# Performance work log

Hardware: AMD Instinct MI355X
Metric: run time of the kernel (lower is better)

## Reference

```python
import jax, jax.numpy as jnp
import numpy as np

H = 1024
N_HEADS = 16
DK = H // N_HEADS
B = 4
S_TGT = 1024
S_SRC = 1024
LN_EPS = 1e-5


def _ln(x, g, b):
    m = jnp.mean(x, axis=-1, keepdims=True)
    v = jnp.mean(jnp.square(x - m), axis=-1, keepdims=True)
    return (x - m) * jax.lax.rsqrt(v + LN_EPS) * g + b


def _mha(q_in, k_in, v_in, wq, wk, wv, wo, mask):
    # Equivalent to torch split(hidden//n_splits)+cat(dim=0) head layout:
    # per-(batch,head) scaled dot-product attention.
    Bq, Sq, _ = q_in.shape
    Sk = k_in.shape[1]
    q = (q_in @ wq).reshape(Bq, Sq, N_HEADS, DK)
    k = (k_in @ wk).reshape(Bq, Sk, N_HEADS, DK)
    v = (v_in @ wv).reshape(Bq, Sk, N_HEADS, DK)
    scores = jnp.einsum('bqhd,bkhd->bhqk', q, k)
    if mask is not None:
        scores = jnp.where(mask[:, None, :, :], -jnp.inf, scores)
    attn = jax.nn.softmax(scores / np.sqrt(DK).astype(np.float32), axis=-1)
    ctx = jnp.einsum('bhqk,bkhd->bqhd', attn, v).reshape(Bq, Sq, H)
    return ctx @ wo


def setup_inputs() -> dict:
    key = jax.random.key(0)
    ks = jax.random.split(key, 16)
    std = 1.0 / np.sqrt(H)
    p = {
        'x': jax.random.normal(ks[0], (B, S_TGT, H), jnp.float32),
        'key_and_value': jax.random.normal(ks[1], (B, S_SRC, H), jnp.float32),
        'mask': jnp.zeros((B, S_TGT, S_SRC), jnp.bool_),  # no padding
        # causal mask: True above the diagonal (masked positions)
        'future_mask': jnp.broadcast_to(
            jnp.triu(jnp.ones((S_TGT, S_TGT), jnp.bool_), k=1), (B, S_TGT, S_TGT)),
        'sa_wq': jax.random.normal(ks[2], (H, H), jnp.float32) * std,
        'sa_wk': jax.random.normal(ks[3], (H, H), jnp.float32) * std,
        'sa_wv': jax.random.normal(ks[4], (H, H), jnp.float32) * std,
        'sa_wo': jax.random.normal(ks[5], (H, H), jnp.float32) * std,
        'ca_wq': jax.random.normal(ks[6], (H, H), jnp.float32) * std,
        'ca_wk': jax.random.normal(ks[7], (H, H), jnp.float32) * std,
        'ca_wv': jax.random.normal(ks[8], (H, H), jnp.float32) * std,
        'ca_wo': jax.random.normal(ks[9], (H, H), jnp.float32) * std,
        'fc_w1': jax.random.normal(ks[10], (H, 4 * H), jnp.float32) * std,
        'fc_b1': jnp.zeros((4 * H,), jnp.float32),
        'fc_w2': jax.random.normal(ks[11], (4 * H, H), jnp.float32) * (0.5 * std),
        'fc_b2': jnp.zeros((H,), jnp.float32),
        'ln1_g': jnp.ones((H,), jnp.float32), 'ln1_b': jnp.zeros((H,), jnp.float32),
        'ln2_g': jnp.ones((H,), jnp.float32), 'ln2_b': jnp.zeros((H,), jnp.float32),
        'ln3_g': jnp.ones((H,), jnp.float32), 'ln3_b': jnp.zeros((H,), jnp.float32),
    }
    return p


def reference(x, key_and_value, mask, future_mask,
              sa_wq, sa_wk, sa_wv, sa_wo,
              ca_wq, ca_wk, ca_wv, ca_wo,
              fc_w1, fc_b1, fc_w2, fc_b2,
              ln1_g, ln1_b, ln2_g, ln2_b, ln3_g, ln3_b):
    # prev is None path (training); dropout in eval mode = identity.
    z = _ln(x, ln1_g, ln1_b)
    z = x + _mha(z, z, z, sa_wq, sa_wk, sa_wv, sa_wo, future_mask)
    nkv = _ln(key_and_value, ln2_g, ln2_b)
    z = z + _mha(_ln(z, ln2_g, ln2_b), nkv, nkv, ca_wq, ca_wk, ca_wv, ca_wo, mask)
    h = jax.nn.relu(_ln(z, ln3_g, ln3_b) @ fc_w1 + fc_b1)
    z = z + (h @ fc_w2 + fc_b2)
    return z
```

## Files before the change

kernel.cpp:

```cpp
#include <hip/hip_runtime.h>
#include <hip/hip_bf16.h>

typedef __attribute__((ext_vector_type(8))) short short8;
typedef __attribute__((ext_vector_type(4))) float f32x4;
using bf16 = __hip_bfloat16;

__device__ __forceinline__ void gload16(const void* g, void* l) {
  __builtin_amdgcn_global_load_lds(
      (const __attribute__((address_space(1))) void*)g,
      (__attribute__((address_space(3))) void*)l, 16, 0, 0);
}

__device__ __forceinline__ short f2bf(float f) {
  bf16 h = __float2bfloat16(f);
  short s;
  __builtin_memcpy(&s, &h, 2);
  return s;
}

__global__ __launch_bounds__(256)
void wtr8(const float* w0, const float* w1, const float* w2, const float* w3,
          const float* w4, const float* w5, const float* w6, const float* w7,
          bf16* __restrict__ Wout) {
  __shared__ float tile[32][33];
  const float* w;
  switch (blockIdx.z) {
    case 0: w = w0; break; case 1: w = w1; break;
    case 2: w = w2; break; case 3: w = w3; break;
    case 4: w = w4; break; case 5: w = w5; break;
    case 6: w = w6; break; default: w = w7; break;
  }
  bf16* wt = Wout + (size_t)blockIdx.z * 1024 * 1024;
  const int tx = threadIdx.x & 31, ty = threadIdx.x >> 5;
  const int c0 = blockIdx.x * 32, r0 = blockIdx.y * 32;
#pragma unroll
  for (int i = 0; i < 4; ++i)
    tile[ty * 4 + i][tx] = w[(size_t)(r0 + ty * 4 + i) * 1024 + c0 + tx];
  __syncthreads();
#pragma unroll
  for (int i = 0; i < 4; ++i) {
    const int cc = ty * 4 + i;
    wt[(size_t)(c0 + cc) * 1024 + r0 + tx] = __float2bfloat16(tile[tx][cc]);
  }
}

__global__ __launch_bounds__(256)
void wtr(const float* __restrict__ w, bf16* __restrict__ wt, int R, int C) {
  __shared__ float tile[32][33];
  const int tx = threadIdx.x & 31, ty = threadIdx.x >> 5;
  const int c0 = blockIdx.x * 32, r0 = blockIdx.y * 32;
#pragma unroll
  for (int i = 0; i < 4; ++i)
    tile[ty * 4 + i][tx] = w[(size_t)(r0 + ty * 4 + i) * C + c0 + tx];
  __syncthreads();
#pragma unroll
  for (int i = 0; i < 4; ++i) {
    const int cc = ty * 4 + i;
    wt[(size_t)(c0 + cc) * R + r0 + tx] = __float2bfloat16(tile[tx][cc]);
  }
}

__global__ __launch_bounds__(256)
void ln_k(const float* __restrict__ x, const float* __restrict__ g,
          const float* __restrict__ b, bf16* __restrict__ y) {
  const int row = blockIdx.x, t = threadIdx.x;
  const int wv = t >> 6, l = t & 63;
  const float4 v = reinterpret_cast<const float4*>(x + (size_t)row * 1024)[t];
  float s = v.x + v.y + v.z + v.w;
  float s2 = v.x * v.x + v.y * v.y + v.z * v.z + v.w * v.w;
#pragma unroll
  for (int m = 1; m < 64; m <<= 1) {
    s += __shfl_xor(s, m, 64);
    s2 += __shfl_xor(s2, m, 64);
  }
  __shared__ float ps[4], ps2[4];
  if (l == 0) { ps[wv] = s; ps2[wv] = s2; }
  __syncthreads();
  s = ps[0] + ps[1] + ps[2] + ps[3];
  s2 = ps2[0] + ps2[1] + ps2[2] + ps2[3];
  const float mean = s * (1.f / 1024.f);
  const float var = s2 * (1.f / 1024.f) - mean * mean;
  const float rs = rsqrtf(var + 1e-5f);
  const float4 gg = reinterpret_cast<const float4*>(g)[t];
  const float4 bb = reinterpret_cast<const float4*>(b)[t];
  ushort4 o;
  o.x = (unsigned short)f2bf((v.x - mean) * rs * gg.x + bb.x);
  o.y = (unsigned short)f2bf((v.y - mean) * rs * gg.y + bb.y);
  o.z = (unsigned short)f2bf((v.z - mean) * rs * gg.z + bb.z);
  o.w = (unsigned short)f2bf((v.w - mean) * rs * gg.w + bb.w);
  reinterpret_cast<ushort4*>(y + (size_t)row * 1024)[t] = o;
}

template <int BM, int EPI>
__global__ __launch_bounds__(256, 2)
void gemm_bt(const bf16* __restrict__ A, const bf16* __restrict__ BT,
             const float* bias, const float* res, void* outp,
             int M, int N, int K, bf16* vtp, int nv0) {
  constexpr int WM = BM / 32;
  constexpr int APASS = BM / 32;
  __shared__ alignas(16) short al[2][BM * 64];
  __shared__ alignas(16) short bl[2][128 * 64];
  const int t = threadIdx.x;
  const int gx = N >> 7;
  const int nwg = gridDim.x * gridDim.y;
  int id = blockIdx.y * gridDim.x + blockIdx.x;
  id = (id & 7) * (nwg >> 3) + (id >> 3);
  const int bx = id % gx, by = id / gx;
  const int m0 = by * BM, n0 = bx * 128;
  const int wv = t >> 6, l = t & 63, lr = l & 15, lk = l >> 4;
  const int wr = wv >> 1, wc = wv & 1;
  const int tr = t >> 3, tc = (t & 7) * 8;
  const int tcs = (((t & 7) ^ (tr & 7)) * 8);
  const int cro0 = ((lk ^ (lr & 7)) * 8);
  const int cro1 = (((4 + lk) ^ (lr & 7)) * 8);

  f32x4 acc[WM][4];
#pragma unroll
  for (int i = 0; i < WM; ++i)
#pragma unroll
    for (int j = 0; j < 4; ++j) acc[i][j] = (f32x4)0.f;

#define STAGE(buf, k0)                                                        \
  do {                                                                        \
    _Pragma("unroll") for (int it = 0; it < APASS; ++it) {                    \
      const int row = it * 32 + tr;                                           \
      gload16(A + (size_t)(m0 + row) * K + (k0) + tcs,                        \
              (char*)&al[buf][row * 64 + tc]);                                \
    }                                                                         \
    _Pragma("unroll") for (int it = 0; it < 4; ++it) {                        \
      const int row = it * 32 + tr;                                           \
      gload16(BT + (size_t)(n0 + row) * K + (k0) + tcs,                       \
              (char*)&bl[buf][row * 64 + tc]);                                \
    }                                                                         \
  } while (0)

#define COMPUTE(cur)                                                          \
  do {                                                                        \
    _Pragma("unroll") for (int ks = 0; ks < 2; ++ks) {                        \
      const int cro = ks ? cro1 : cro0;                                       \
      short8 af[WM], bfv[4];                                                  \
      _Pragma("unroll") for (int m = 0; m < WM; ++m) af[m] =                  \
          *reinterpret_cast<const short8*>(                                   \
              &al[cur][(wr * (BM / 2) + m * 16 + lr) * 64 + cro]);            \
      _Pragma("unroll") for (int n = 0; n < 4; ++n) bfv[n] =                  \
          *reinterpret_cast<const short8*>(                                   \
              &bl[cur][(wc * 64 + n * 16 + lr) * 64 + cro]);                  \
      _Pragma("unroll") for (int m = 0; m < WM; ++m)                          \
          _Pragma("unroll") for (int n = 0; n < 4; ++n) acc[m][n] =           \
              __builtin_amdgcn_mfma_f32_16x16x32_bf16(af[m], bfv[n],          \
                                                      acc[m][n], 0, 0, 0);    \
    }                                                                         \
  } while (0)

  const int nt = K >> 6;
  if constexpr (BM == 64) {
    STAGE(0, 0);
    STAGE(1, 64);
    for (int tk = 0; tk < nt; ++tk) {
      const int cur = tk & 1;
      if (tk < nt - 1)
        asm volatile("s_waitcnt vmcnt(6)" ::: "memory");
      else
        asm volatile("s_waitcnt vmcnt(0)" ::: "memory");
      __builtin_amdgcn_s_barrier();
      COMPUTE(cur);
      if (tk + 2 < nt) {
        asm volatile("s_waitcnt lgkmcnt(0)" ::: "memory");
        __builtin_amdgcn_s_barrier();
        STAGE(cur, (tk + 2) << 6);
      }
    }
  } else {
    STAGE(0, 0);
    asm volatile("s_waitcnt vmcnt(0)" ::: "memory");
    __syncthreads();
    for (int tk = 0; tk < nt; ++tk) {
      const int cur = tk & 1;
      if (tk + 1 < nt) STAGE(cur ^ 1, (tk + 1) << 6);
      COMPUTE(cur);
      asm volatile("s_waitcnt vmcnt(0)" ::: "memory");
      __syncthreads();
    }
  }
#undef STAGE
#undef COMPUTE

  const int r0 = m0 + wr * (BM / 2), c0 = n0 + wc * 64;
  if constexpr (EPI == 4) {
#pragma unroll
    for (int m = 0; m < WM; ++m) {
      const int rowb = r0 + m * 16 + lk * 4;
      const int bb = rowb >> 10, s0 = rowb & 1023;
#pragma unroll
      for (int n = 0; n < 4; ++n) {
        const int col = c0 + n * 16 + lr;
        if (col < nv0) {
#pragma unroll
          for (int r = 0; r < 4; ++r)
            ((bf16*)outp)[(size_t)(rowb + r) * nv0 + col] =
                __float2bfloat16(acc[m][n][r]);
        } else {
          ushort4 u;
          u.x = (unsigned short)f2bf(acc[m][n][0]);
          u.y = (unsigned short)f2bf(acc[m][n][1]);
          u.z = (unsigned short)f2bf(acc[m][n][2]);
          u.w = (unsigned short)f2bf(acc[m][n][3]);
          const size_t vidx = ((size_t)bb * 1024 + (col - nv0)) * 1024 + s0;
          *reinterpret_cast<ushort4*>(vtp + vidx) = u;
        }
      }
    }
  } else {
#pragma unroll
    for (int m = 0; m < WM; ++m)
#pragma unroll
      for (int n = 0; n < 4; ++n) {
        const int col = c0 + n * 16 + lr;
#pragma unroll
        for (int r = 0; r < 4; ++r) {
          const int row = r0 + m * 16 + lk * 4 + r;
          const size_t idx = (size_t)row * N + col;
          float v = acc[m][n][r];
          if (EPI == 0) {
            ((bf16*)outp)[idx] = __float2bfloat16(v);
          } else if (EPI == 1) {
            ((float*)outp)[idx] = res[idx] + v;
          } else if (EPI == 2) {
            v += bias[col];
            ((bf16*)outp)[idx] = __float2bfloat16(fmaxf(v, 0.f));
          } else {
            ((float*)outp)[idx] = res[idx] + v + bias[col];
          }
        }
      }
  }
}

template <bool CAUSAL>
__global__ __launch_bounds__(256, 2)
void flash8(const bf16* __restrict__ Qb, int ldq,
            const bf16* __restrict__ Kb, int ldk,
            const bf16* __restrict__ VTb, bf16* __restrict__ Ob) {
  __shared__ alignas(16) short kl[3][64 * 64];
  __shared__ alignas(16) short vl[3][64 * 64];
  __shared__ alignas(16) short pl[4][32 * 72];
  const int t = threadIdx.x, wv = t >> 6, l = t & 63, lr = l & 15, lk = l >> 4;
  const int raw = blockIdx.y * 8 + blockIdx.x;
  const int id = (raw & 7) * 64 + (raw >> 3);
  const int qb = id & 7, bh = id >> 3;
  const int b = bh >> 4, h = bh & 15;
  const size_t rowbase = (size_t)b * 1024;
  const int q0 = qb * 128 + wv * 32;
  const bf16* Vbase = VTb + (rowbase + h * 64) * 1024;

  const int tr = t >> 3;
  const int tcd = (t & 7) * 8;
  const int tcs = (((t & 7) ^ (tr & 7)) * 8);
  const int cro0 = ((lk ^ (lr & 7)) * 8);
  const int cro1 = (((4 + lk) ^ (lr & 7)) * 8);

  short8 qf[2][2];
#pragma unroll
  for (int m = 0; m < 2; ++m)
#pragma unroll
    for (int ks = 0; ks < 2; ++ks)
      qf[m][ks] = *reinterpret_cast<const short8*>(
          Qb + (rowbase + q0 + m * 16 + lr) * ldq + h * 64 + ks * 32 + lk * 8);

  short8 ones;
#pragma unroll
  for (int j = 0; j < 8; ++j) ones[j] = (short)0x3F80;

  f32x4 accO[2][4];
  f32x4 accL[2];
#pragma unroll
  for (int m = 0; m < 2; ++m) {
#pragma unroll
    for (int n = 0; n < 4; ++n) accO[m][n] = (f32x4)0.f;
    accL[m] = (f32x4)0.f;
  }

  const int ntb = CAUSAL ? (qb * 2 + 2) : 16;
  const int myLast = q0 >> 6;

#define FSTAGE(buf, kv0)                                                      \
  do {                                                                        \
    _Pragma("unroll") for (int it = 0; it < 2; ++it) {                        \
      const int row = it * 32 + tr;                                           \
      gload16(Kb + (rowbase + (kv0) + row) * ldk + h * 64 + tcs,              \
              (char*)&kl[buf][row * 64 + tcd]);                               \
    }                                                                         \
    _Pragma("unroll") for (int it = 0; it < 2; ++it) {                        \
      const int row = it * 32 + tr;                                           \
      gload16(Vbase + (size_t)row * 1024 + (kv0) + tcs,                       \
              (char*)&vl[buf][row * 64 + tcd]);                               \
    }                                                                         \
  } while (0)

  FSTAGE(0, 0);
  FSTAGE(1, 64);
  int cur = 0;
  for (int tk = 0; tk < ntb; ++tk) {
    if (tk < ntb - 1)
      asm volatile("s_waitcnt vmcnt(4)" ::: "memory");
    else
      asm volatile("s_waitcnt vmcnt(0)" ::: "memory");
    __builtin_amdgcn_s_barrier();
    if (tk + 2 < ntb) {
      int stg = cur + 2;
      if (stg >= 3) stg -= 3;
      FSTAGE(stg, (tk + 2) << 6);
    }
    if (!CAUSAL || tk <= myLast) {
      const int kv0 = tk * 64;
      const bool needmask = CAUSAL && (tk == myLast);
      f32x4 sa[2][4];
#pragma unroll
      for (int m = 0; m < 2; ++m)
#pragma unroll
        for (int n = 0; n < 4; ++n) sa[m][n] = (f32x4)0.f;
#pragma unroll
      for (int ks = 0; ks < 2; ++ks) {
        const int cro = ks ? cro1 : cro0;
        short8 kf[4];
#pragma unroll
        for (int n = 0; n < 4; ++n)
          kf[n] = *reinterpret_cast<const short8*>(
              &kl[cur][(n * 16 + lr) * 64 + cro]);
        __builtin_amdgcn_s_setprio(1);
#pragma unroll
        for (int m = 0; m < 2; ++m)
#pragma unroll
          for (int n = 0; n < 4; ++n)
            sa[m][n] = __builtin_amdgcn_mfma_f32_16x16x32_bf16(
                qf[m][ks], kf[n], sa[m][n], 0, 0, 0);
        __builtin_amdgcn_s_setprio(0);
      }
#pragma unroll
      for (int m = 0; m < 2; ++m) {
#pragma unroll
        for (int r = 0; r < 4; ++r) {
          const int row = q0 + m * 16 + lk * 4 + r;
          float s0 = sa[m][0][r] * 0.125f, s1 = sa[m][1][r] * 0.125f;
          float s2 = sa[m][2][r] * 0.125f, s3 = sa[m][3][r] * 0.125f;
          if (needmask) {
            if (kv0 + 0 + lr > row) s0 = -1e30f;
            if (kv0 + 16 + lr > row) s1 = -1e30f;
            if (kv0 + 32 + lr > row) s2 = -1e30f;
            if (kv0 + 48 + lr > row) s3 = -1e30f;
          }
          const float p0 = __expf(s0), p1 = __expf(s1);
          const float p2 = __expf(s2), p3 = __expf(s3);
          const int prow = m * 16 + lk * 4 + r;
          pl[wv][prow * 72 + lr + 0] = f2bf(p0);
          pl[wv][prow * 72 + lr + 16] = f2bf(p1);
          pl[wv][prow * 72 + lr + 32] = f2bf(p2);
          pl[wv][prow * 72 + lr + 48] = f2bf(p3);
        }
      }
#pragma unroll
      for (int ks = 0; ks < 2; ++ks) {
        const int cro = ks ? cro1 : cro0;
        short8 pf[2], vf[4];
#pragma unroll
        for (int m = 0; m < 2; ++m)
          pf[m] = *reinterpret_cast<const short8*>(
              &pl[wv][(m * 16 + lr) * 72 + ks * 32 + lk * 8]);
#pragma unroll
        for (int n = 0; n < 4; ++n)
          vf[n] = *reinterpret_cast<const short8*>(
              &vl[cur][(n * 16 + lr) * 64 + cro]);
        __builtin_amdgcn_s_setprio(1);
#pragma unroll
        for (int m = 0; m < 2; ++m) {
#pragma unroll
          for (int n = 0; n < 4; ++n)
            accO[m][n] = __builtin_amdgcn_mfma_f32_16x16x32_bf16(
                pf[m], vf[n], accO[m][n], 0, 0, 0);
          accL[m] = __builtin_amdgcn_mfma_f32_16x16x32_bf16(
              pf[m], ones, accL[m], 0, 0, 0);
        }
        __builtin_amdgcn_s_setprio(0);
      }
    }
    cur = (cur + 1 == 3) ? 0 : cur + 1;
  }
#undef FSTAGE

#pragma unroll
  for (int m = 0; m < 2; ++m)
#pragma unroll
    for (int n = 0; n < 4; ++n)
#pragma unroll
      for (int r = 0; r < 4; ++r) {
        const int row = q0 + m * 16 + lk * 4 + r;
        const int col = n * 16 + lr;
        const float o = accO[m][n][r] / accL[m][r];
        Ob[(rowbase + row) * 1024 + h * 64 + col] = __float2bfloat16(o);
      }
}

extern "C" void kernel_launch(void* const* d_in, const int* in_sizes, int n_in,
                              void* d_out, int out_size, void* d_ws,
                              size_t ws_size, hipStream_t stream) {
  const float* x = (const float*)d_in[0];
  const float* kv_in = (const float*)d_in[1];
  const float* sa_wq = (const float*)d_in[4];
  const float* sa_wk = (const float*)d_in[5];
  const float* sa_wv = (const float*)d_in[6];
  const float* sa_wo = (const float*)d_in[7];
  const float* ca_wq = (const float*)d_in[8];
  const float* ca_wk = (const float*)d_in[9];
  const float* ca_wv = (const float*)d_in[10];
  const float* ca_wo = (const float*)d_in[11];
  const float* fc_w1 = (const float*)d_in[12];
  const float* fc_b1 = (const float*)d_in[13];
  const float* fc_w2 = (const float*)d_in[14];
  const float* fc_b2 = (const float*)d_in[15];
  const float* ln1_g = (const float*)d_in[16];
  const float* ln1_b = (const float*)d_in[17];
  const float* ln2_g = (const float*)d_in[18];
  const float* ln2_b = (const float*)d_in[19];
  const float* ln3_g = (const float*)d_in[20];
  const float* ln3_b = (const float*)d_in[21];

  char* ws = (char*)d_ws;
  const size_t MB = 1024 * 1024;
  bf16* W = (bf16*)ws;
  bf16* w1T = W + 8 * MB;
  bf16* w2T = W + 12 * MB;
  float* z = (float*)(ws + 32 * MB);
  bf16* t0 = (bf16*)(ws + 48 * MB);
  bf16* qkvb = (bf16*)(ws + 56 * MB);
  bf16* vts = (bf16*)(ws + 72 * MB);
  bf16* kb = (bf16*)(ws + 80 * MB);
  bf16* vtc = (bf16*)(ws + 88 * MB);
  bf16* qb = (bf16*)(ws + 96 * MB);
  bf16* ctx = (bf16*)(ws + 104 * MB);
  bf16* kvln = (bf16*)(ws + 112 * MB);
  bf16* hb = (bf16*)(ws + 120 * MB);

  const dim3 B256(256);
  wtr8<<<dim3(32, 32, 8), B256, 0, stream>>>(sa_wq, sa_wk, sa_wv, sa_wo,
                                             ca_wq, ca_wk, ca_wv, ca_wo, W);
  wtr<<<dim3(128, 32), B256, 0, stream>>>(fc_w1, w1T, 1024, 4096);
  wtr<<<dim3(32, 128), B256, 0, stream>>>(fc_w2, w2T, 4096, 1024);

  ln_k<<<4096, B256, 0, stream>>>(x, ln1_g, ln1_b, t0);
  gemm_bt<128, 4><<<dim3(24, 32), B256, 0, stream>>>(
      t0, W, nullptr, nullptr, qkvb, 4096, 3072, 1024, vts, 2048);
  flash8<true><<<dim3(8, 64), B256, 0, stream>>>(
      qkvb, 2048, qkvb + 1024, 2048, vts, ctx);
  gemm_bt<64, 1><<<dim3(8, 64), B256, 0, stream>>>(
      ctx, W + 3 * MB, nullptr, x, z, 4096, 1024, 1024, nullptr, 0);

  ln_k<<<4096, B256, 0, stream>>>(kv_in, ln2_g, ln2_b, kvln);
  ln_k<<<4096, B256, 0, stream>>>(z, ln2_g, ln2_b, t0);
  gemm_bt<128, 4><<<dim3(16, 32), B256, 0, stream>>>(
      kvln, W + 5 * MB, nullptr, nullptr, kb, 4096, 2048, 1024, vtc, 1024);
  gemm_bt<64, 0><<<dim3(8, 64), B256, 0, stream>>>(
      t0, W + 4 * MB, nullptr, nullptr, qb, 4096, 1024, 1024, nullptr, 0);
  flash8<false><<<dim3(8, 64), B256, 0, stream>>>(
      qb, 1024, kb, 1024, vtc, ctx);
  gemm_bt<64, 1><<<dim3(8, 64), B256, 0, stream>>>(
      ctx, W + 7 * MB, nullptr, z, z, 4096, 1024, 1024, nullptr, 0);

  ln_k<<<4096, B256, 0, stream>>>(z, ln3_g, ln3_b, t0);
  gemm_bt<128, 2><<<dim3(32, 32), B256, 0, stream>>>(
      t0, w1T, fc_b1, nullptr, hb, 4096, 4096, 1024, nullptr, 0);
  gemm_bt<64, 3><<<dim3(8, 64), B256, 0, stream>>>(
      hb, w2T, fc_b2, z, d_out, 4096, 1024, 4096, nullptr, 0);
}
```

Measured before the change: 360.0 us.

## Split-K the second FFN GEMM and unify double-buffered GEMM pipeline

The FC2 GEMM (K=4096) now runs as a split-K over two halves via blockIdx.z, each writing fp32 partials. A new elementwise kernel sums the partials with the residual and bias. This raises wave count and parallelism for the long-K GEMM. The BM=128 GEMM path also switches to the two-stage prefetch pipeline used by BM=64, with a matching vmcnt. The cost is extra fp32 partial traffic plus one more kernel launch.

```diff
diff --git a/kernel.cpp b/kernel.cpp
--- a/kernel.cpp
+++ b/kernel.cpp
@@ -91,13 +91,29 @@
   reinterpret_cast<ushort4*>(y + (size_t)row * 1024)[t] = o;
 }
 
+__global__ __launch_bounds__(256)
+void ffn_add(const float4* __restrict__ p0, const float4* __restrict__ p1,
+             const float4* __restrict__ res, const float4* __restrict__ bias,
+             float4* __restrict__ out) {
+  const size_t i = (size_t)blockIdx.x * 256 + threadIdx.x;
+  const float4 a = p0[i], b = p1[i], r = res[i];
+  const float4 g = bias[i & 255];
+  float4 o;
+  o.x = a.x + b.x + r.x + g.x;
+  o.y = a.y + b.y + r.y + g.y;
+  o.z = a.z + b.z + r.z + g.z;
+  o.w = a.w + b.w + r.w + g.w;
+  out[i] = o;
+}
+
 template <int BM, int EPI>
 __global__ __launch_bounds__(256, 2)
 void gemm_bt(const bf16* __restrict__ A, const bf16* __restrict__ BT,
              const float* bias, const float* res, void* outp,
-             int M, int N, int K, bf16* vtp, int nv0) {
+             int M, int N, int K, int lda, bf16* vtp, int nv0) {
   constexpr int WM = BM / 32;
   constexpr int APASS = BM / 32;
+  constexpr int NLD = APASS + 4;
   __shared__ alignas(16) short al[2][BM * 64];
   __shared__ alignas(16) short bl[2][128 * 64];
   const int t = threadIdx.x;
@@ -114,6 +130,9 @@
   const int cro0 = ((lk ^ (lr & 7)) * 8);
   const int cro1 = (((4 + lk) ^ (lr & 7)) * 8);
 
+  const bf16* Ab = (EPI == 5) ? A + (size_t)blockIdx.z * K : A;
+  const bf16* BTb = (EPI == 5) ? BT + (size_t)blockIdx.z * K : BT;
+
   f32x4 acc[WM][4];
 #pragma unroll
   for (int i = 0; i < WM; ++i)
@@ -124,12 +143,12 @@
   do {                                                                        \
     _Pragma("unroll") for (int it = 0; it < APASS; ++it) {                    \
       const int row = it * 32 + tr;                                           \
-      gload16(A + (size_t)(m0 + row) * K + (k0) + tcs,                        \
+      gload16(Ab + (size_t)(m0 + row) * lda + (k0) + tcs,                     \
               (char*)&al[buf][row * 64 + tc]);                                \
     }                                                                         \
     _Pragma("unroll") for (int it = 0; it < 4; ++it) {                        \
       const int row = it * 32 + tr;                                           \
-      gload16(BT + (size_t)(n0 + row) * K + (k0) + tcs,                       \
+      gload16(BTb + (size_t)(n0 + row) * lda + (k0) + tcs,                    \
               (char*)&bl[buf][row * 64 + tc]);                                \
     }                                                                         \
   } while (0)
@@ -153,33 +172,24 @@
   } while (0)
 
   const int nt = K >> 6;
-  if constexpr (BM == 64) {
-    STAGE(0, 0);
-    STAGE(1, 64);
-    for (int tk = 0; tk < nt; ++tk) {
-      const int cur = tk & 1;
-      if (tk < nt - 1)
+  STAGE(0, 0);
+  STAGE(1, 64);
+  for (int tk = 0; tk < nt; ++tk) {
+    const int cur = tk & 1;
+    if (tk < nt - 1) {
+      if constexpr (NLD == 6)
         asm volatile("s_waitcnt vmcnt(6)" ::: "memory");
       else
-        asm volatile("s_waitcnt vmcnt(0)" ::: "memory");
+        asm volatile("s_waitcnt vmcnt(8)" ::: "memory");
+    } else {
+      asm volatile("s_waitcnt vmcnt(0)" ::: "memory");
+    }
+    __builtin_amdgcn_s_barrier();
+    COMPUTE(cur);
+    if (tk + 2 < nt) {
+      asm volatile("s_waitcnt lgkmcnt(0)" ::: "memory");
       __builtin_amdgcn_s_barrier();
-      COMPUTE(cur);
-      if (tk + 2 < nt) {
-        asm volatile("s_waitcnt lgkmcnt(0)" ::: "memory");
-        __builtin_amdgcn_s_barrier();
-        STAGE(cur, (tk + 2) << 6);
-      }
-    }
-  } else {
-    STAGE(0, 0);
-    asm volatile("s_waitcnt vmcnt(0)" ::: "memory");
-    __syncthreads();
-    for (int tk = 0; tk < nt; ++tk) {
-      const int cur = tk & 1;
-      if (tk + 1 < nt) STAGE(cur ^ 1, (tk + 1) << 6);
-      COMPUTE(cur);
-      asm volatile("s_waitcnt vmcnt(0)" ::: "memory");
-      __syncthreads();
+      STAGE(cur, (tk + 2) << 6);
     }
   }
 #undef STAGE
@@ -211,6 +221,8 @@
       }
     }
   } else {
+    float* po5 = nullptr;
+    if constexpr (EPI == 5) po5 = blockIdx.z ? (float*)vtp : (float*)outp;
 #pragma unroll
     for (int m = 0; m < WM; ++m)
 #pragma unroll
@@ -228,8 +240,10 @@
           } else if (EPI == 2) {
             v += bias[col];
             ((bf16*)outp)[idx] = __float2bfloat16(fmaxf(v, 0.f));
+          } else if (EPI == 3) {
+            ((float*)outp)[idx] = res[idx] + v + bias[col];
           } else {
-            ((float*)outp)[idx] = res[idx] + v + bias[col];
+            po5[idx] = v;
           }
         }
       }
@@ -439,6 +453,8 @@
   bf16* ctx = (bf16*)(ws + 104 * MB);
   bf16* kvln = (bf16*)(ws + 112 * MB);
   bf16* hb = (bf16*)(ws + 120 * MB);
+  float* part0 = (float*)(ws + 56 * MB);
+  float* part1 = (float*)(ws + 80 * MB);
 
   const dim3 B256(256);
   wtr8<<<dim3(32, 32, 8), B256, 0, stream>>>(sa_wq, sa_wk, sa_wv, sa_wo,
@@ -448,26 +464,32 @@
 
   ln_k<<<4096, B256, 0, stream>>>(x, ln1_g, ln1_b, t0);
   gemm_bt<128, 4><<<dim3(24, 32), B256, 0, stream>>>(
-      t0, W, nullptr, nullptr, qkvb, 4096, 3072, 1024, vts, 2048);
+      t0, W, nullptr, nullptr, qkvb, 4096, 3072, 1024, 1024, vts, 2048);
   flash8<true><<<dim3(8, 64), B256, 0, stream>>>(
       qkvb, 2048, qkvb + 1024, 2048, vts, ctx);
   gemm_bt<64, 1><<<dim3(8, 64), B256, 0, stream>>>(
-      ctx, W + 3 * MB, nullptr, x, z, 4096, 1024, 1024, nullptr, 0);
+      ctx, W + 3 * MB, nullptr, x, z, 4096, 1024, 1024, 1024, nullptr, 0);
 
   ln_k<<<4096, B256, 0, stream>>>(kv_in, ln2_g, ln2_b, kvln);
   ln_k<<<4096, B256, 0, stream>>>(z, ln2_g, ln2_b, t0);
   gemm_bt<128, 4><<<dim3(16, 32), B256, 0, stream>>>(
-      kvln, W + 5 * MB, nullptr, nullptr, kb, 4096, 2048, 1024, vtc, 1024);
+      kvln, W + 5 * MB, nullptr, nullptr, kb, 4096, 2048, 1024, 1024, vtc,
+      1024);
   gemm_bt<64, 0><<<dim3(8, 64), B256, 0, stream>>>(
-      t0, W + 4 * MB, nullptr, nullptr, qb, 4096, 1024, 1024, nullptr, 0);
+      t0, W + 4 * MB, nullptr, nullptr, qb, 4096, 1024, 1024, 1024, nullptr,
+      0);
   flash8<false><<<dim3(8, 64), B256, 0, stream>>>(
       qb, 1024, kb, 1024, vtc, ctx);
   gemm_bt<64, 1><<<dim3(8, 64), B256, 0, stream>>>(
-      ctx, W + 7 * MB, nullptr, z, z, 4096, 1024, 1024, nullptr, 0);
+      ctx, W + 7 * MB, nullptr, z, z, 4096, 1024, 1024, 1024, nullptr, 0);
 
   ln_k<<<4096, B256, 0, stream>>>(z, ln3_g, ln3_b, t0);
   gemm_bt<128, 2><<<dim3(32, 32), B256, 0, stream>>>(
-      t0, w1T, fc_b1, nullptr, hb, 4096, 4096, 1024, nullptr, 0);
-  gemm_bt<64, 3><<<dim3(8, 64), B256, 0, stream>>>(
-      hb, w2T, fc_b2, z, d_out, 4096, 1024, 4096, nullptr, 0);
-}
+      t0, w1T, fc_b1, nullptr, hb, 4096, 4096, 1024, 1024, nullptr, 0);
+  gemm_bt<64, 5><<<dim3(8, 64, 2), B256, 0, stream>>>(
+      hb, w2T, nullptr, nullptr, part0, 4096, 1024, 2048, 4096,
+      (bf16*)part1, 0);
+  ffn_add<<<4096, B256, 0, stream>>>(
+      (const float4*)part0, (const float4*)part1, (const float4*)z,
+      (const float4*)fc_b2, (float4*)d_out);
+}
```

Result: slower. 373.6 us (+3.8%).

## Add 256x256-tile 512-thread GEMM kernel for FFN first layer

Applied to the files above, without the earlier changes.

Adds a dedicated 256x256 output-tile GEMM with 512 threads, XOR-swizzled LDS, double-buffered direct-to-LDS loads and a fused bias+ReLU bf16 epilogue, and uses it for the FC1 projection (4096x4096x1024) in place of the 128-tile generic kernel. Larger tiles raise arithmetic intensity and cut global and LDS traffic per MFMA. The cost is a 256-block grid on a large-CU GPU, which is roughly one wave of work with one block per CU, plus high register and LDS pressure.

```diff
diff --git a/kernel.cpp b/kernel.cpp
--- a/kernel.cpp
+++ b/kernel.cpp
@@ -234,6 +234,100 @@
         }
       }
   }
+}
+
+__global__ __launch_bounds__(512, 1)
+void gemm256(const bf16* __restrict__ A, const bf16* __restrict__ BT,
+             const float* __restrict__ bias, bf16* __restrict__ outp,
+             int M, int N, int K) {
+  __shared__ alignas(16) short al[2][256 * 64];
+  __shared__ alignas(16) short bl[2][256 * 64];
+  const int t = threadIdx.x;
+  const int gx = N >> 8;
+  const int nwg = gridDim.x * gridDim.y;
+  int id = blockIdx.y * gridDim.x + blockIdx.x;
+  id = (id & 7) * (nwg >> 3) + (id >> 3);
+  const int bx = id % gx, by = id / gx;
+  const int m0 = by * 256, n0 = bx * 256;
+  const int wid = t >> 6, l = t & 63, lr = l & 15, lk = l >> 4;
+  const int wm = wid >> 2, wn = wid & 3;
+  const int tr = t >> 3, tc = (t & 7) * 8;
+  const int tcs = (((t & 7) ^ (tr & 7)) * 8);
+  const int cro0 = ((lk ^ (lr & 7)) * 8);
+  const int cro1 = (((4 + lk) ^ (lr & 7)) * 8);
+
+  f32x4 acc[8][4];
+#pragma unroll
+  for (int i = 0; i < 8; ++i)
+#pragma unroll
+    for (int j = 0; j < 4; ++j) acc[i][j] = (f32x4)0.f;
+
+#define STAGE2(buf, k0)                                                       \
+  do {                                                                        \
+    _Pragma("unroll") for (int it = 0; it < 4; ++it) {                        \
+      const int row = it * 64 + tr;                                           \
+      gload16(A + (size_t)(m0 + row) * K + (k0) + tcs,                        \
+              (char*)&al[buf][row * 64 + tc]);                                \
+    }                                                                         \
+    _Pragma("unroll") for (int it = 0; it < 4; ++it) {                        \
+      const int row = it * 64 + tr;                                           \
+      gload16(BT + (size_t)(n0 + row) * K + (k0) + tcs,                       \
+              (char*)&bl[buf][row * 64 + tc]);                                \
+    }                                                                         \
+  } while (0)
+
+#define COMPUTE2(cur)                                                         \
+  do {                                                                        \
+    _Pragma("unroll") for (int ks = 0; ks < 2; ++ks) {                        \
+      const int cro = ks ? cro1 : cro0;                                       \
+      short8 af[8], bfv[4];                                                   \
+      _Pragma("unroll") for (int m = 0; m < 8; ++m) af[m] =                   \
+          *reinterpret_cast<const short8*>(                                   \
+              &al[cur][(wm * 128 + m * 16 + lr) * 64 + cro]);                 \
+      _Pragma("unroll") for (int n = 0; n < 4; ++n) bfv[n] =                  \
+          *reinterpret_cast<const short8*>(                                   \
+              &bl[cur][(wn * 64 + n * 16 + lr) * 64 + cro]);                  \
+      _Pragma("unroll") for (int m = 0; m < 8; ++m)                           \
+          _Pragma("unroll") for (int n = 0; n < 4; ++n) acc[m][n] =           \
+              __builtin_amdgcn_mfma_f32_16x16x32_bf16(af[m], bfv[n],          \
+                                                      acc[m][n], 0, 0, 0);    \
+    }                                                                         \
+  } while (0)
+
+  const int nt = K >> 6;
+  STAGE2(0, 0);
+  STAGE2(1, 64);
+  for (int tk = 0; tk < nt; ++tk) {
+    const int cur = tk & 1;
+    if (tk < nt - 1)
+      asm volatile("s_waitcnt vmcnt(8)" ::: "memory");
+    else
+      asm volatile("s_waitcnt vmcnt(0)" ::: "memory");
+    __builtin_amdgcn_s_barrier();
+    COMPUTE2(cur);
+    if (tk + 2 < nt) {
+      asm volatile("s_waitcnt lgkmcnt(0)" ::: "memory");
+      __builtin_amdgcn_s_barrier();
+      STAGE2(cur, (tk + 2) << 6);
+    }
+  }
+#undef STAGE2
+#undef COMPUTE2
+
+  const int r0 = m0 + wm * 128, c0 = n0 + wn * 64;
+#pragma unroll
+  for (int m = 0; m < 8; ++m)
+#pragma unroll
+    for (int n = 0; n < 4; ++n) {
+      const int col = c0 + n * 16 + lr;
+      const float bcol = bias[col];
+#pragma unroll
+      for (int r = 0; r < 4; ++r) {
+        const int row = r0 + m * 16 + lk * 4 + r;
+        const float v = acc[m][n][r] + bcol;
+        outp[(size_t)row * N + col] = __float2bfloat16(fmaxf(v, 0.f));
+      }
+    }
 }
 
 template <bool CAUSAL>
@@ -466,8 +560,8 @@
       ctx, W + 7 * MB, nullptr, z, z, 4096, 1024, 1024, nullptr, 0);
 
   ln_k<<<4096, B256, 0, stream>>>(z, ln3_g, ln3_b, t0);
-  gemm_bt<128, 2><<<dim3(32, 32), B256, 0, stream>>>(
-      t0, w1T, fc_b1, nullptr, hb, 4096, 4096, 1024, nullptr, 0);
+  gemm256<<<dim3(16, 16), dim3(512), 0, stream>>>(
+      t0, w1T, fc_b1, hb, 4096, 4096, 1024);
   gemm_bt<64, 3><<<dim3(8, 64), B256, 0, stream>>>(
       hb, w2T, fc_b2, z, d_out, 4096, 1024, 4096, nullptr, 0);
 }
```

Result: faster. 335.5 us (-6.8%).
